# Kernel optimization log

Measured on AMD Instinct MI355X. Metric: run time of the kernel, lower is better.

The kernel has to match this reference:

```python
import jax, jax.numpy as jnp
import numpy as np

D_MODEL = 256
N_LAYERS = 4
D_STATE = 16
EXPAND = 2
D_CONV = 4
D_INNER = EXPAND * D_MODEL
DT_RANK = (D_MODEL + 15) // 16  # ceil(d_model/16) = 16
BATCH = 8
SEQ = 2048
EPS = 1e-5


def setup_inputs() -> dict:
    key = jax.random.key(0)
    ks = jax.random.split(key, 12)
    rn = lambda k, s, sc=0.02: jax.random.normal(k, s, dtype=jnp.float32) * sc
    A_log = jnp.log(jnp.broadcast_to(jnp.arange(1, D_STATE + 1, dtype=jnp.float32),
                                     (N_LAYERS, D_INNER, D_STATE)))
    return {
        "x": jax.random.normal(ks[0], (BATCH, SEQ, 2), dtype=jnp.float32),
        "w_in": rn(ks[1], (D_MODEL, 2), 0.5),
        "b_in": jnp.zeros((D_MODEL,), jnp.float32),
        "norm_w": jnp.ones((N_LAYERS, D_MODEL), jnp.float32),
        "in_proj_w": rn(ks[2], (N_LAYERS, 2 * D_INNER, D_MODEL)),
        "conv_w": rn(ks[3], (N_LAYERS, D_INNER, 1, D_CONV), 0.1),
        "conv_b": jnp.zeros((N_LAYERS, D_INNER), jnp.float32),
        "x_proj_w": rn(ks[4], (N_LAYERS, DT_RANK + 2 * D_STATE, D_INNER)),
        "dt_proj_w": rn(ks[5], (N_LAYERS, D_INNER, DT_RANK), 0.1),
        "dt_proj_b": rn(ks[6], (N_LAYERS, D_INNER), 0.1),
        "A_log": A_log,
        "D_skip": jnp.ones((N_LAYERS, D_INNER), jnp.float32),
        "out_proj_w": rn(ks[7], (N_LAYERS, D_MODEL, D_INNER)),
        "w_head": rn(ks[8], (1, D_MODEL), 0.1),
        "b_head": jnp.zeros((1,), jnp.float32),
    }


def _rmsnorm(x, w):
    return x * jax.lax.rsqrt(jnp.mean(x * x, axis=-1, keepdims=True) + EPS) * w


def _causal_dw_conv(x, w, b):
    # x: (B, L, C); w: (C, 1, K) depthwise; causal left-pad K-1
    xt = jnp.swapaxes(x, 1, 2)  # (B, C, L)
    y = jax.lax.conv_general_dilated(xt, w, (1,), [(D_CONV - 1, 0)],
                                     dimension_numbers=("NCH", "OIH", "NCH"),
                                     feature_group_count=D_INNER)
    return jnp.swapaxes(y + b[None, :, None], 1, 2)


def _selective_scan(u, delta, A, Bm, Cm, Dp):
    # u, delta: (B, L, E); A: (E, N); Bm, Cm: (B, L, N); Dp: (E,)
    dA = jnp.exp(delta[..., None] * A)                 # (B, L, E, N)
    dBu = (delta * u)[..., None] * Bm[:, :, None, :]   # (B, L, E, N)

    def step(h, t):
        dA_t, dBu_t = t
        h = dA_t * h + dBu_t
        return h, h

    h0 = jnp.zeros((u.shape[0], A.shape[0], A.shape[1]), u.dtype)
    _, hs = jax.lax.scan(step, h0, (jnp.swapaxes(dA, 0, 1), jnp.swapaxes(dBu, 0, 1)))
    y = jnp.einsum("lben,bln->ble", hs, Cm)            # (B, L, E)
    return y + u * Dp


def _mamba_block(x, in_w, cw, cb, xp_w, dtw, dtb, A_log, Dp, out_w):
    xz = x @ in_w.T                                    # (B, L, 2E)
    u, z = jnp.split(xz, 2, axis=-1)
    u = jax.nn.silu(_causal_dw_conv(u, cw, cb))
    dbc = u @ xp_w.T                                   # (B, L, dt_rank + 2N)
    delta = jax.nn.softplus(dbc[..., :DT_RANK] @ dtw.T + dtb)
    Bm = dbc[..., DT_RANK:DT_RANK + D_STATE]
    Cm = dbc[..., DT_RANK + D_STATE:]
    y = _selective_scan(u, delta, -jnp.exp(A_log), Bm, Cm, Dp)
    return (y * jax.nn.silu(z)) @ out_w.T


def reference(x, w_in, b_in, norm_w, in_proj_w, conv_w, conv_b, x_proj_w,
              dt_proj_w, dt_proj_b, A_log, D_skip, out_proj_w, w_head, b_head):
    h = x @ w_in.T + b_in                              # (B, L, d_model)
    for i in range(N_LAYERS):
        h = h + _mamba_block(_rmsnorm(h, norm_w[i]), in_proj_w[i], conv_w[i],
                             conv_b[i], x_proj_w[i], dt_proj_w[i], dt_proj_b[i],
                             A_log[i], D_skip[i], out_proj_w[i])
    return (h @ w_head.T + b_head)[..., 0]             # (B, L)
```

## Files before the change

### kernel.cpp

```cpp
#include <hip/hip_runtime.h>
#include <hip/hip_bf16.h>

#define BATCH 8
#define SEQ   2048
#define DM    256
#define DI    512
#define DS    16
#define DTR   16
#define NL    4
#define ROWS  (BATCH*SEQ)
#define NCH   32
#define CHL   64
#define NF    576

typedef __attribute__((ext_vector_type(8))) __bf16 bh8;
typedef __attribute__((ext_vector_type(4))) float f4;

#if __has_builtin(__builtin_amdgcn_exp2f)
#define EXP2(x) __builtin_amdgcn_exp2f(x)
#else
#define EXP2(x) exp2f(x)
#endif
#define LOG2E 1.4426950408889634f

__device__ __forceinline__ float bf2f(unsigned short u) {
    union { unsigned int i; float f; } v; v.i = ((unsigned int)u) << 16; return v.f;
}
__device__ __forceinline__ float4 us4f(ushort4 q) {
    return make_float4(bf2f(q.x), bf2f(q.y), bf2f(q.z), bf2f(q.w));
}
__device__ __forceinline__ float ldg1(const void* p, int i, int bf) {
    if (bf) return bf2f(((const unsigned short*)p)[i]);
    return ((const float*)p)[i];
}
__device__ __forceinline__ float4 ldg4(const void* p, int i, int bf) {
    if (bf) return us4f(*(const ushort4*)(((const unsigned short*)p) + i));
    return *(const float4*)(((const float*)p) + i);
}
__device__ __forceinline__ unsigned short f2bs(float f) {
    union { float f; unsigned u; } x; x.f = f;
    unsigned r = (x.u + 0x7fffu + ((x.u >> 16) & 1u)) >> 16;
    return (unsigned short)r;
}
__device__ __forceinline__ float fsilu(float x) {
    return x * __builtin_amdgcn_rcpf(1.0f + __expf(-x));
}
__device__ __forceinline__ float fsoftplus(float x) {
    return (x > 15.0f) ? x : __logf(1.0f + __expf(x));
}
__device__ __forceinline__ void pow16(float e1, float* pw) {
    float p2 = e1 * e1, p3 = p2 * e1, p4 = p2 * p2;
    float p5 = p4 * e1, p6 = p4 * p2, p7 = p4 * p3, p8 = p4 * p4;
    pw[0] = e1; pw[1] = p2; pw[2] = p3; pw[3] = p4;
    pw[4] = p5; pw[5] = p6; pw[6] = p7; pw[7] = p8;
    pw[8]  = p8 * e1; pw[9]  = p8 * p2; pw[10] = p8 * p3; pw[11] = p8 * p4;
    pw[12] = p8 * p5; pw[13] = p8 * p6; pw[14] = p8 * p7; pw[15] = p8 * p8;
}

typedef const __attribute__((address_space(1))) unsigned int* gas_t;
typedef __attribute__((address_space(3))) unsigned int* las_t;
__device__ __forceinline__ void gl16(const void* g, void* l) {
    __builtin_amdgcn_global_load_lds((gas_t)g, (las_t)l, 16, 0, 0);
}

__global__ void k_probe(const void* x, const void* A_log, int* flag) {
    int t = threadIdx.x;
    float v = bf2f(((const unsigned short*)x)[2 * t]);
    int bad = (fabsf(v) < 32.0f) ? 0 : 1;
    for (int o = 1; o < 64; o <<= 1) bad += __shfl_xor(bad, o);
    int bf = (bad > 8) ? 0 : 1;
    int nb = 0;
    for (int j = 0; j < 64; j++) {
        int e = ((j * 64 + t) * 17) & 32767;
        int n = e & 15;
        float a = ldg1(A_log, e, bf);
        float ea = __expf(a);
        if (fabsf(ea - (float)(n + 1)) > 0.02f * (float)(n + 1)) nb = 1;
    }
    for (int o = 1; o < 64; o <<= 1) nb += __shfl_xor(nb, o);
    if (t == 0) { flag[0] = bf; flag[1] = (nb == 0) ? 1 : 0; }
}

__global__ __launch_bounds__(256) void k_prep(const void* dtw, const void* xpw,
                                              unsigned short* Wc, const int* flag) {
    int bf = *flag;
    int blk = blockIdx.x;
    int l = blk / NF, r = blk % NF;
    int t = threadIdx.x;
    unsigned short* out = Wc + ((size_t)l * NF + r) * DI;
#pragma unroll
    for (int p = 0; p < 2; p++) {
        int k = t + p * 256;
        float v = 0.0f;
        if (r < 512) {
            const int db = l * DI * DTR + r * DTR;
            const int xb = l * 48 * DI;
#pragma unroll
            for (int j = 0; j < 16; j++)
                v = fmaf(ldg1(dtw, db + j, bf), ldg1(xpw, xb + j * DI + k, bf), v);
        } else if (r < 544) {
            v = ldg1(xpw, l * 48 * DI + (16 + r - 512) * DI + k, bf);
        }
        out[k] = f2bs(v);
    }
}

__global__ __launch_bounds__(256) void k_prepw(const void* ipw, const void* norm_w,
                                               unsigned short* Wip, const int* flag) {
    int bf = *flag;
    int blk = blockIdx.x;
    int l = blk >> 10, r = blk & 1023;
    int t = threadIdx.x;
    float v = ldg1(ipw, (l * 1024 + r) * 256 + t, bf) * ldg1(norm_w, l * 256 + t, bf);
    Wip[((size_t)l * 1024 + r) * 256 + t] = f2bs(v);
}

__global__ __launch_bounds__(256) void k_inproj(const void* x, const void* w_in, const void* b_in,
                                                unsigned short* h, float* rssq, const int* flag) {
    int bf = *flag;
    int row = blockIdx.x, e = threadIdx.x;
    float x0 = ldg1(x, row * 2 + 0, bf), x1 = ldg1(x, row * 2 + 1, bf);
    float w0 = ldg1(w_in, e * 2 + 0, bf), w1 = ldg1(w_in, e * 2 + 1, bf);
    float bb = ldg1(b_in, e, bf);
    unsigned short hb = f2bs(fmaf(x0, w0, fmaf(x1, w1, bb)));
    h[(size_t)row * DM + e] = hb;
    float hv = bf2f(hb);
    float ss = hv * hv;
#pragma unroll
    for (int o = 1; o < 64; o <<= 1) ss += __shfl_xor(ss, o);
    if ((e & 63) == 0) rssq[(size_t)row * 4 + (e >> 6)] = ss;
}

#define ASTR 72

template <int BN, bool ADD, bool SCALE, bool RSUM, bool WINT>
__global__ __launch_bounds__(256, 4) void k_mfma(const unsigned short* A, const void* W, int w_off,
                                                 unsigned short* Cp, float* rssq,
                                                 int N, int K, const int* flag) {
    int bf = *flag;
    __shared__ unsigned short SMEM[(128 + BN) * ASTR];
    unsigned short* As = SMEM;
    unsigned short* Ws = SMEM + 128 * 64;
    constexpr int NT = BN / 32;
    constexpr int TSTR = BN + 8;

    int bm = blockIdx.x, bn = blockIdx.y;
    int t = threadIdx.x;
    int w = t >> 6, lane = t & 63;
    int wm = w >> 1, wn = w & 1;
    int lr = lane & 15, quad = lane >> 4;
    int crow = lane >> 3;
    int ccol = ((lane & 7) ^ (lane >> 3)) * 8;

    f4 acc[4][NT];
#pragma unroll
    for (int i = 0; i < 4; i++)
#pragma unroll
        for (int j = 0; j < NT; j++) acc[i][j] = f4{0.f, 0.f, 0.f, 0.f};

    for (int k0 = 0; k0 < K; k0 += 64) {
        __syncthreads();
#pragma unroll
        for (int i = 0; i < 4; i++) {
            int ci = w * 4 + i;
            int r = ci * 8 + crow;
            gl16(A + (size_t)(bm * 128 + r) * K + k0 + ccol, &As[ci * 512]);
        }
        if (WINT || bf) {
#pragma unroll
            for (int i = 0; i < BN / 32; i++) {
                int ci = w * (BN / 32) + i;
                int r = ci * 8 + crow;
                gl16((const unsigned short*)W + (size_t)w_off +
                         (size_t)(bn * BN + r) * K + k0 + ccol,
                     &Ws[ci * 512]);
            }
        } else {
#pragma unroll
            for (int i = 0; i < BN * 8 / 256; i++) {
                int ch = t + i * 256;
                int r = ch >> 3, kc = (ch & 7) * 8;
                size_t off = (size_t)w_off + (size_t)(bn * BN + r) * K + k0 + kc;
                const float* src = (const float*)W + off;
                float4 a0 = *(const float4*)src;
                float4 a1 = *(const float4*)(src + 4);
                ushort4 v0 = { f2bs(a0.x), f2bs(a0.y), f2bs(a0.z), f2bs(a0.w) };
                ushort4 v1 = { f2bs(a1.x), f2bs(a1.y), f2bs(a1.z), f2bs(a1.w) };
                unsigned short* dst = &Ws[r * 64 + (kc ^ ((r & 7) << 3))];
                *(ushort4*)dst = v0;
                *(ushort4*)(dst + 4) = v1;
            }
        }
        __syncthreads();
#pragma unroll
        for (int ks = 0; ks < 64; ks += 32) {
            int csw = (ks + quad * 8) ^ ((lr & 7) << 3);
            bh8 af[4];
#pragma unroll
            for (int i = 0; i < 4; i++)
                af[i] = *(const bh8*)&As[(wm * 64 + i * 16 + lr) * 64 + csw];
            bh8 wf[NT];
#pragma unroll
            for (int j = 0; j < NT; j++)
                wf[j] = *(const bh8*)&Ws[(wn * (BN / 2) + j * 16 + lr) * 64 + csw];
#pragma unroll
            for (int i = 0; i < 4; i++)
#pragma unroll
                for (int j = 0; j < NT; j++)
                    acc[i][j] = __builtin_amdgcn_mfma_f32_16x16x32_bf16(af[i], wf[j], acc[i][j], 0, 0, 0);
        }
    }
    __syncthreads();
    unsigned short* Tile = SMEM;
#pragma unroll
    for (int i = 0; i < 4; i++) {
        int rl = wm * 64 + i * 16 + quad * 4;
        float sc4[4];
        if (SCALE) {
#pragma unroll
            for (int r = 0; r < 4; r++) {
                float4 q4 = *(const float4*)&rssq[(size_t)(bm * 128 + rl + r) * 4];
                sc4[r] = rsqrtf((q4.x + q4.y + q4.z + q4.w) * (1.0f / (float)DM) + 1e-5f);
            }
        }
#pragma unroll
        for (int j = 0; j < NT; j++) {
            int cl = wn * (BN / 2) + j * 16 + lr;
#pragma unroll
            for (int r = 0; r < 4; r++) {
                float vv = acc[i][j][r];
                if (SCALE) vv *= sc4[r];
                Tile[(rl + r) * TSTR + cl] = f2bs(vv);
            }
        }
    }
    __syncthreads();
    constexpr int CPT = 128 * BN / 8 / 256;
#pragma unroll
    for (int i = 0; i < CPT; i++) {
        int ch = t + i * 256;
        int r = ch / (BN / 8), qc = (ch % (BN / 8)) * 8;
        uint4 v = *(uint4*)&Tile[r * TSTR + qc];
        size_t gidx = (size_t)(bm * 128 + r) * N + bn * BN + qc;
        if (ADD) {
            uint4 c = *(uint4*)&Cp[gidx];
            unsigned short* vp = (unsigned short*)&v;
            unsigned short* cp2 = (unsigned short*)&c;
            uint4 ov;
            unsigned short* op = (unsigned short*)&ov;
            float ssq = 0.0f;
#pragma unroll
            for (int e = 0; e < 8; e++) {
                op[e] = f2bs(bf2f(vp[e]) + bf2f(cp2[e]));
                if (RSUM) { float hv = bf2f(op[e]); ssq = fmaf(hv, hv, ssq); }
            }
            *(uint4*)&Cp[gidx] = ov;
            if (RSUM) {
#pragma unroll
                for (int o2 = 1; o2 < 8; o2 <<= 1) ssq += __shfl_xor(ssq, o2);
                if ((lane & 7) == 0) rssq[(size_t)(bm * 128 + r) * 4 + bn] = ssq;
            }
        } else {
            *(uint4*)&Cp[gidx] = v;
        }
    }
}

__global__ __launch_bounds__(256, 4) void k_fused(const unsigned short* A, const unsigned short* Wc,
                                                  int w_off, unsigned short* delta, float* BC,
                                                  const void* dtb, int layer, const int* flag) {
    int bf = *flag;
    __shared__ unsigned short SMEM[(128 + 64) * ASTR];
    unsigned short* As = SMEM;
    unsigned short* Ws = SMEM + 128 * 64;
    constexpr int TSTR = 72;

    int bm = blockIdx.x, bn = blockIdx.y;
    int t = threadIdx.x;
    int w = t >> 6, lane = t & 63;
    int wm = w >> 1, wn = w & 1;
    int lr = lane & 15, quad = lane >> 4;
    int crow = lane >> 3;
    int ccol = ((lane & 7) ^ (lane >> 3)) * 8;

    f4 acc[4][2];
#pragma unroll
    for (int i = 0; i < 4; i++)
#pragma unroll
        for (int j = 0; j < 2; j++) acc[i][j] = f4{0.f, 0.f, 0.f, 0.f};

    for (int k0 = 0; k0 < DI; k0 += 64) {
        __syncthreads();
#pragma unroll
        for (int i = 0; i < 4; i++) {
            int ci = w * 4 + i;
            int r = ci * 8 + crow;
            gl16(A + (size_t)(bm * 128 + r) * DI + k0 + ccol, &As[ci * 512]);
        }
#pragma unroll
        for (int i = 0; i < 2; i++) {
            int ci = w * 2 + i;
            int r = ci * 8 + crow;
            gl16(Wc + (size_t)w_off + (size_t)(bn * 64 + r) * DI + k0 + ccol, &Ws[ci * 512]);
        }
        __syncthreads();
#pragma unroll
        for (int ks = 0; ks < 64; ks += 32) {
            int csw = (ks + quad * 8) ^ ((lr & 7) << 3);
            bh8 af[4];
#pragma unroll
            for (int i = 0; i < 4; i++)
                af[i] = *(const bh8*)&As[(wm * 64 + i * 16 + lr) * 64 + csw];
            bh8 wf[2];
#pragma unroll
            for (int j = 0; j < 2; j++)
                wf[j] = *(const bh8*)&Ws[(wn * 32 + j * 16 + lr) * 64 + csw];
#pragma unroll
            for (int i = 0; i < 4; i++)
#pragma unroll
                for (int j = 0; j < 2; j++)
                    acc[i][j] = __builtin_amdgcn_mfma_f32_16x16x32_bf16(af[i], wf[j], acc[i][j], 0, 0, 0);
        }
    }
    if (bn < 8) {
        __syncthreads();
        unsigned short* Tile = SMEM;
#pragma unroll
        for (int i = 0; i < 4; i++) {
            int rl = wm * 64 + i * 16 + quad * 4;
#pragma unroll
            for (int j = 0; j < 2; j++) {
                int cl = wn * 32 + j * 16 + lr;
                float bb = ldg1(dtb, layer * DI + bn * 64 + cl, bf);
#pragma unroll
                for (int r = 0; r < 4; r++)
                    Tile[(rl + r) * TSTR + cl] = f2bs(fsoftplus(acc[i][j][r] + bb));
            }
        }
        __syncthreads();
#pragma unroll
        for (int i = 0; i < 4; i++) {
            int ch = t + i * 256;
            int r = ch >> 3, qc = (ch & 7) * 8;
            uint4 v = *(uint4*)&Tile[r * TSTR + qc];
            *(uint4*)&delta[(size_t)(bm * 128 + r) * DI + bn * 64 + qc] = v;
        }
    } else {
#pragma unroll
        for (int i = 0; i < 4; i++) {
            int row0 = bm * 128 + wm * 64 + i * 16 + quad * 4;
#pragma unroll
            for (int j = 0; j < 2; j++) {
                int col = bn * 64 + wn * 32 + j * 16 + lr;
                if (col < 544) {
#pragma unroll
                    for (int r = 0; r < 4; r++)
                        BC[(size_t)(row0 + r) * 32 + (col - 512)] = acc[i][j][r];
                }
            }
        }
    }
}

__global__ __launch_bounds__(256) void k_conv(const unsigned short* xz, const void* cw, const void* cb,
                                              int layer, unsigned short* u, const int* flag) {
    int bf = *flag;
    int idx = blockIdx.x * 256 + threadIdx.x;
    int dq = idx & 127;
    int row = idx >> 7;
    int l = row & (SEQ - 1);
    int d = dq * 4;
    float4 w0 = ldg4(cw, (layer * DI + d + 0) * 4, bf);
    float4 w1 = ldg4(cw, (layer * DI + d + 1) * 4, bf);
    float4 w2 = ldg4(cw, (layer * DI + d + 2) * 4, bf);
    float4 w3 = ldg4(cw, (layer * DI + d + 3) * 4, bf);
    float4 bb = ldg4(cb, layer * DI + d, bf);
    const unsigned short* base = xz + (size_t)row * (2 * DI) + d;
    float4 t0 = make_float4(0, 0, 0, 0), t1 = t0, t2 = t0;
    if (l >= 3) t0 = us4f(*(const ushort4*)(base - 3 * 2 * DI));
    if (l >= 2) t1 = us4f(*(const ushort4*)(base - 2 * 2 * DI));
    if (l >= 1) t2 = us4f(*(const ushort4*)(base - 1 * 2 * DI));
    float4 t3 = us4f(*(const ushort4*)base);
    float a0 = bb.x; a0 = fmaf(w0.x, t0.x, a0); a0 = fmaf(w0.y, t1.x, a0); a0 = fmaf(w0.z, t2.x, a0); a0 = fmaf(w0.w, t3.x, a0);
    float a1 = bb.y; a1 = fmaf(w1.x, t0.y, a1); a1 = fmaf(w1.y, t1.y, a1); a1 = fmaf(w1.z, t2.y, a1); a1 = fmaf(w1.w, t3.y, a1);
    float a2 = bb.z; a2 = fmaf(w2.x, t0.z, a2); a2 = fmaf(w2.y, t1.z, a2); a2 = fmaf(w2.z, t2.z, a2); a2 = fmaf(w2.w, t3.z, a2);
    float a3 = bb.w; a3 = fmaf(w3.x, t0.w, a3); a3 = fmaf(w3.y, t1.w, a3); a3 = fmaf(w3.z, t2.w, a3); a3 = fmaf(w3.w, t3.w, a3);
    ushort4 o = { f2bs(fsilu(a0)), f2bs(fsilu(a1)), f2bs(fsilu(a2)), f2bs(fsilu(a3)) };
    *(ushort4*)(u + (size_t)row * DI + d) = o;
}

__global__ __launch_bounds__(256) void k_scan1(const unsigned short* delta, const unsigned short* u,
                                               const float* BC, const void* A_log, float* Sb, float* E,
                                               int layer, const int* flag) {
    int bf = flag[0], sA = flag[1];
    int x = blockIdx.x;
    int dg = x & 1, c = (x >> 1) & (NCH - 1), b = x >> 6;
    int tid = threadIdx.x;
    int d = dg * 256 + tid;
    int t0 = c * CHL;

    __shared__ float sB[CHL][16];
    {
        int r = tid >> 2, q = tid & 3;
        *(float4*)&sB[r][q * 4] =
            *(const float4*)(BC + ((size_t)b * SEQ + t0 + r) * 32 + q * 4);
    }

    float A2[16];
#pragma unroll
    for (int n4 = 0; n4 < 4; n4++) {
        float4 a4 = ldg4(A_log, (layer * DI + d) * DS + n4 * 4, bf);
        A2[n4 * 4 + 0] = -__expf(a4.x) * LOG2E;
        A2[n4 * 4 + 1] = -__expf(a4.y) * LOG2E;
        A2[n4 * 4 + 2] = -__expf(a4.z) * LOG2E;
        A2[n4 * 4 + 3] = -__expf(a4.w) * LOG2E;
    }
    float h[16];
#pragma unroll
    for (int n = 0; n < 16; n++) h[n] = 0.0f;
    float S = 0.0f;

    const unsigned short* dp = delta + ((size_t)b * SEQ + t0) * DI + d;
    const unsigned short* up = u + ((size_t)b * SEQ + t0) * DI + d;

    float dl0[4], uu0[4];
#pragma unroll
    for (int j = 0; j < 4; j++) { dl0[j] = bf2f(dp[j * DI]); uu0[j] = bf2f(up[j * DI]); }
    __syncthreads();

    for (int s = 0; s < CHL / 4; s++) {
        int sn = (s + 1 < CHL / 4) ? (s + 1) : s;
        float dl1[4], uu1[4];
#pragma unroll
        for (int j = 0; j < 4; j++) {
            dl1[j] = bf2f(dp[(sn * 4 + j) * DI]);
            uu1[j] = bf2f(up[(sn * 4 + j) * DI]);
        }
#pragma unroll
        for (int j = 0; j < 4; j++) {
            int t = s * 4 + j;
            float dlt = dl0[j], uu = uu0[j];
            float du = dlt * uu;
            S += dlt;
            if (sA) {
                float pw[16];
                pow16(EXP2(-dlt * LOG2E), pw);
#pragma unroll
                for (int n4 = 0; n4 < 4; n4++) {
                    float4 Bv = *(const float4*)&sB[t][n4 * 4];
                    int n = n4 * 4;
                    h[n + 0] = fmaf(pw[n + 0], h[n + 0], du * Bv.x);
                    h[n + 1] = fmaf(pw[n + 1], h[n + 1], du * Bv.y);
                    h[n + 2] = fmaf(pw[n + 2], h[n + 2], du * Bv.z);
                    h[n + 3] = fmaf(pw[n + 3], h[n + 3], du * Bv.w);
                }
            } else {
#pragma unroll
                for (int n4 = 0; n4 < 4; n4++) {
                    float4 Bv = *(const float4*)&sB[t][n4 * 4];
                    int n = n4 * 4;
                    float a0 = EXP2(dlt * A2[n + 0]); h[n + 0] = fmaf(a0, h[n + 0], du * Bv.x);
                    float a1 = EXP2(dlt * A2[n + 1]); h[n + 1] = fmaf(a1, h[n + 1], du * Bv.y);
                    float a2 = EXP2(dlt * A2[n + 2]); h[n + 2] = fmaf(a2, h[n + 2], du * Bv.z);
                    float a3 = EXP2(dlt * A2[n + 3]); h[n + 3] = fmaf(a3, h[n + 3], du * Bv.w);
                }
            }
        }
#pragma unroll
        for (int j = 0; j < 4; j++) { dl0[j] = dl1[j]; uu0[j] = uu1[j]; }
    }
    Sb[((size_t)b * NCH + c) * DI + d] = S;
    float* Ed = E + (((size_t)b * NCH + c) * DI + d) * DS;
#pragma unroll
    for (int n4 = 0; n4 < 4; n4++)
        *(float4*)(Ed + n4 * 4) = make_float4(h[n4 * 4], h[n4 * 4 + 1], h[n4 * 4 + 2], h[n4 * 4 + 3]);
}

__global__ __launch_bounds__(256) void k_stitch(const float* Sb, const void* A_log, float* E,
                                                int layer, const int* flag) {
    int bf = flag[0];
    int g = blockIdx.x * 256 + threadIdx.x;
    int b = g >> 13, r = g & 8191;
    int d = r >> 4;
    float A2a = -__expf(ldg1(A_log, (layer * DI + d) * DS + (r & 15), bf)) * LOG2E;
    size_t ebase = (size_t)b * NCH * (DI * DS) + r;
    float H = 0.0f;
    for (int c = 0; c < NCH; c++) {
        float p = EXP2(A2a * Sb[((size_t)b * NCH + c) * DI + d]);
        size_t idx = ebase + (size_t)c * (DI * DS);
        float e = E[idx];
        E[idx] = H;
        H = fmaf(p, H, e);
    }
}

__global__ __launch_bounds__(256) void k_scan2(const unsigned short* delta, const unsigned short* u,
                                               const float* BC, const void* A_log, const void* D_skip,
                                               const unsigned short* xz, const float* E,
                                               unsigned short* g, int layer, const int* flag) {
    int bf = flag[0], sA = flag[1];
    int x = blockIdx.x;
    int dg = x & 1, c = (x >> 1) & (NCH - 1), b = x >> 6;
    int tid = threadIdx.x;
    int d = dg * 256 + tid;
    int t0 = c * CHL;

    __shared__ float sBC[CHL][32];
#pragma unroll
    for (int k2 = 0; k2 < 2; k2++) {
        int fi = k2 * 256 + tid;
        int r = fi >> 3, q = fi & 7;
        *(float4*)&sBC[r][q * 4] =
            *(const float4*)(BC + ((size_t)b * SEQ + t0 + r) * 32 + q * 4);
    }

    float A2[16];
#pragma unroll
    for (int n4 = 0; n4 < 4; n4++) {
        float4 a4 = ldg4(A_log, (layer * DI + d) * DS + n4 * 4, bf);
        A2[n4 * 4 + 0] = -__expf(a4.x) * LOG2E;
        A2[n4 * 4 + 1] = -__expf(a4.y) * LOG2E;
        A2[n4 * 4 + 2] = -__expf(a4.z) * LOG2E;
        A2[n4 * 4 + 3] = -__expf(a4.w) * LOG2E;
    }
    float Dp = ldg1(D_skip, layer * DI + d, bf);

    float h[16];
    const float* E0 = E + (((size_t)b * NCH + c) * DI + d) * DS;
#pragma unroll
    for (int n4 = 0; n4 < 4; n4++) {
        float4 h4 = *(const float4*)(E0 + n4 * 4);
        h[n4 * 4 + 0] = h4.x; h[n4 * 4 + 1] = h4.y; h[n4 * 4 + 2] = h4.z; h[n4 * 4 + 3] = h4.w;
    }

    const unsigned short* dp = delta + ((size_t)b * SEQ + t0) * DI + d;
    const unsigned short* up = u + ((size_t)b * SEQ + t0) * DI + d;
    const unsigned short* zp = xz + ((size_t)b * SEQ + t0) * (2 * DI) + DI + d;
    unsigned short* gp = g + ((size_t)b * SEQ + t0) * DI + d;

    float dl0[4], uu0[4], zz0[4];
#pragma unroll
    for (int j = 0; j < 4; j++) {
        dl0[j] = bf2f(dp[j * DI]); uu0[j] = bf2f(up[j * DI]); zz0[j] = bf2f(zp[j * (2 * DI)]);
    }
    __syncthreads();

    for (int s = 0; s < CHL / 4; s++) {
        int sn = (s + 1 < CHL / 4) ? (s + 1) : s;
        float dl1[4], uu1[4], zz1[4];
#pragma unroll
        for (int j = 0; j < 4; j++) {
            dl1[j] = bf2f(dp[(sn * 4 + j) * DI]);
            uu1[j] = bf2f(up[(sn * 4 + j) * DI]);
            zz1[j] = bf2f(zp[(sn * 4 + j) * (2 * DI)]);
        }
#pragma unroll
        for (int j = 0; j < 4; j++) {
            int t = s * 4 + j;
            float dlt = dl0[j], uu = uu0[j], zz = zz0[j];
            float du = dlt * uu;
            float y = 0.0f;
            if (sA) {
                float pw[16];
                pow16(EXP2(-dlt * LOG2E), pw);
#pragma unroll
                for (int n4 = 0; n4 < 4; n4++) {
                    float4 Bv = *(const float4*)&sBC[t][n4 * 4];
                    float4 Cv = *(const float4*)&sBC[t][16 + n4 * 4];
                    int n = n4 * 4;
                    h[n + 0] = fmaf(pw[n + 0], h[n + 0], du * Bv.x); y = fmaf(Cv.x, h[n + 0], y);
                    h[n + 1] = fmaf(pw[n + 1], h[n + 1], du * Bv.y); y = fmaf(Cv.y, h[n + 1], y);
                    h[n + 2] = fmaf(pw[n + 2], h[n + 2], du * Bv.z); y = fmaf(Cv.z, h[n + 2], y);
                    h[n + 3] = fmaf(pw[n + 3], h[n + 3], du * Bv.w); y = fmaf(Cv.w, h[n + 3], y);
                }
            } else {
#pragma unroll
                for (int n4 = 0; n4 < 4; n4++) {
                    float4 Bv = *(const float4*)&sBC[t][n4 * 4];
                    float4 Cv = *(const float4*)&sBC[t][16 + n4 * 4];
                    int n = n4 * 4;
                    float a0 = EXP2(dlt * A2[n + 0]); h[n + 0] = fmaf(a0, h[n + 0], du * Bv.x); y = fmaf(Cv.x, h[n + 0], y);
                    float a1 = EXP2(dlt * A2[n + 1]); h[n + 1] = fmaf(a1, h[n + 1], du * Bv.y); y = fmaf(Cv.y, h[n + 1], y);
                    float a2 = EXP2(dlt * A2[n + 2]); h[n + 2] = fmaf(a2, h[n + 2], du * Bv.z); y = fmaf(Cv.z, h[n + 2], y);
                    float a3 = EXP2(dlt * A2[n + 3]); h[n + 3] = fmaf(a3, h[n + 3], du * Bv.w); y = fmaf(Cv.w, h[n + 3], y);
                }
            }
            float yt = fmaf(uu, Dp, y);
            gp[(size_t)t * DI] = f2bs(yt * fsilu(zz));
        }
#pragma unroll
        for (int j = 0; j < 4; j++) { dl0[j] = dl1[j]; uu0[j] = uu1[j]; zz0[j] = zz1[j]; }
    }
}

__global__ __launch_bounds__(256) void k_head(const unsigned short* h, const void* w_head,
                                              const void* b_head, void* out, const int* flag) {
    int bf = *flag;
    int wv = threadIdx.x >> 6, ln = threadIdx.x & 63;
    int row = blockIdx.x * 4 + wv;
    float4 v = us4f(*(const ushort4*)(h + (size_t)row * DM + ln * 4));
    float4 w = ldg4(w_head, ln * 4, bf);
    float s = v.x * w.x + v.y * w.y + v.z * w.z + v.w * w.w;
    for (int o = 1; o < 64; o <<= 1) s += __shfl_xor(s, o);
    if (ln == 0) {
        s += ldg1(b_head, 0, bf);
        if (bf) ((__hip_bfloat16*)out)[row] = __float2bfloat16(s);
        else    ((float*)out)[row] = s;
    }
}

extern "C" void kernel_launch(void* const* d_in, const int* in_sizes, int n_in,
                              void* d_out, int out_size, void* d_ws, size_t ws_size,
                              hipStream_t stream) {
    (void)in_sizes; (void)n_in; (void)out_size; (void)ws_size;
    const void* x      = d_in[0];
    const void* w_in   = d_in[1];
    const void* b_in   = d_in[2];
    const void* norm_w = d_in[3];
    const void* ipw    = d_in[4];
    const void* cw     = d_in[5];
    const void* cb     = d_in[6];
    const void* xpw    = d_in[7];
    const void* dtw    = d_in[8];
    const void* dtb    = d_in[9];
    const void* A_log  = d_in[10];
    const void* D_skip = d_in[11];
    const void* opw    = d_in[12];
    const void* w_head = d_in[13];
    const void* b_head = d_in[14];

    float* ws    = (float*)d_ws;
    unsigned short* h     = (unsigned short*)ws;
    float*          rssq  = ws + 4194304;
    float*          Sb    = ws + 4194304;
    float*          E     = ws + 4718592;
    unsigned short* xz    = (unsigned short*)(ws + 8388608);
    unsigned short* u     = (unsigned short*)(ws + 25165824);
    float*          BC    = ws + 33554432;
    unsigned short* delta = (unsigned short*)(ws + 34340864);
    unsigned short* Wcomb = (unsigned short*)(ws + 38535168);
    unsigned short* Wipc  = (unsigned short*)(ws + 39124992);
    int*            flag  = (int*)(ws + 42729472);

    k_probe<<<1, 64, 0, stream>>>(x, A_log, flag);
    k_prep<<<NL * NF, 256, 0, stream>>>(dtw, xpw, Wcomb, flag);
    k_prepw<<<NL * 1024, 256, 0, stream>>>(ipw, norm_w, Wipc, flag);
    k_inproj<<<ROWS, 256, 0, stream>>>(x, w_in, b_in, h, rssq, flag);

    for (int layer = 0; layer < NL; layer++) {
        k_mfma<128, false, true, false, true><<<dim3(ROWS / 128, 2 * DI / 128), 256, 0, stream>>>(
            h, Wipc, layer * 2 * DI * DM, xz, rssq, 2 * DI, DM, flag);
        k_conv<<<ROWS * DI / 4 / 256, 256, 0, stream>>>(xz, cw, cb, layer, u, flag);
        k_fused<<<dim3(ROWS / 128, NF / 64), 256, 0, stream>>>(
            u, Wcomb, layer * NF * DI, delta, BC, dtb, layer, flag);
        k_scan1<<<BATCH * NCH * 2, 256, 0, stream>>>(delta, u, BC, A_log, Sb, E, layer, flag);
        k_stitch<<<BATCH * DI * DS / 256, 256, 0, stream>>>(Sb, A_log, E, layer, flag);
        k_scan2<<<BATCH * NCH * 2, 256, 0, stream>>>(delta, u, BC, A_log, D_skip, xz, E,
                                                     u , layer, flag);
        k_mfma<64, true, false, true, false><<<dim3(ROWS / 128, DM / 64), 256, 0, stream>>>(
            u, opw, layer * DM * DI, h, rssq, DM, DI, flag);
    }

    k_head<<<ROWS / 4, 256, 0, stream>>>(h, w_head, b_head, d_out, flag);
}
```

Measured before the change: 587.7 us.

## Fuse causal conv into in-projection GEMM and fold chunk stitch into scan2

The in-projection GEMM now computes the u-half tiles together with 16 extra halo rows, normalizes them with rssq, and applies the depthwise causal conv plus SiLU from shared memory. This removes the separate k_conv pass that re-read xz. The k_stitch kernel is also removed, and each scan2 block recomputes its own starting state by serially combining the earlier chunks' summaries. This costs redundant halo MFMAs and an O(c) prefix loop per block, which is quadratic in chunk count over the whole grid, in exchange for two fewer launches and less global traffic.

```diff
diff --git a/kernel.cpp b/kernel.cpp
--- a/kernel.cpp
+++ b/kernel.cpp
@@ -133,6 +133,155 @@
 
 #define ASTR 72
 
+__global__ __launch_bounds__(256, 4) void k_ipconv(const unsigned short* A, const unsigned short* W,
+                                                   int w_off, unsigned short* xz, unsigned short* u,
+                                                   const float* rssq, const void* cw, const void* cb,
+                                                   int layer, const int* flag) {
+    int bf = *flag;
+    constexpr int K = DM;
+    constexpr int TSTR = 136;
+    __shared__ unsigned short SMEM[144 * TSTR];
+    unsigned short* As  = SMEM;
+    unsigned short* As2 = SMEM + 8192;
+    unsigned short* Ws  = SMEM + 9216;
+
+    int bm = blockIdx.x, bn = blockIdx.y;
+    bool ublk = (bn < 4);
+    int t = threadIdx.x;
+    int w = t >> 6, lane = t & 63;
+    int wm = w >> 1, wn = w & 1;
+    int lr = lane & 15, quad = lane >> 4;
+    int crow = lane >> 3;
+    int ccol = ((lane & 7) ^ (lane >> 3)) * 8;
+
+    f4 acc[4][4];
+    f4 acc5[4];
+#pragma unroll
+    for (int i = 0; i < 4; i++) {
+        acc5[i] = f4{0.f, 0.f, 0.f, 0.f};
+#pragma unroll
+        for (int j = 0; j < 4; j++) acc[i][j] = f4{0.f, 0.f, 0.f, 0.f};
+    }
+
+    for (int k0 = 0; k0 < K; k0 += 64) {
+        __syncthreads();
+#pragma unroll
+        for (int i = 0; i < 4; i++) {
+            int ci = w * 4 + i;
+            int r = ci * 8 + crow;
+            gl16(A + (size_t)(bm * 128 + r) * K + k0 + ccol, &As[ci * 512]);
+        }
+        if (ublk && w < 2) {
+            int rg = bm * 128 - 16 + w * 8 + crow;
+            if (rg < 0) rg = 0;
+            gl16(A + (size_t)rg * K + k0 + ccol, &As2[w * 512]);
+        }
+#pragma unroll
+        for (int i = 0; i < 4; i++) {
+            int ci = w * 4 + i;
+            int r = ci * 8 + crow;
+            gl16(W + (size_t)w_off + (size_t)(bn * 128 + r) * K + k0 + ccol, &Ws[ci * 512]);
+        }
+        __syncthreads();
+#pragma unroll
+        for (int ks = 0; ks < 64; ks += 32) {
+            int csw = (ks + quad * 8) ^ ((lr & 7) << 3);
+            bh8 af[4];
+#pragma unroll
+            for (int i = 0; i < 4; i++)
+                af[i] = *(const bh8*)&As[(wm * 64 + i * 16 + lr) * 64 + csw];
+            bh8 wf[4];
+#pragma unroll
+            for (int j = 0; j < 4; j++)
+                wf[j] = *(const bh8*)&Ws[(wn * 64 + j * 16 + lr) * 64 + csw];
+#pragma unroll
+            for (int i = 0; i < 4; i++)
+#pragma unroll
+                for (int j = 0; j < 4; j++)
+                    acc[i][j] = __builtin_amdgcn_mfma_f32_16x16x32_bf16(af[i], wf[j], acc[i][j], 0, 0, 0);
+            if (ublk && wm == 0) {
+                bh8 a5 = *(const bh8*)&As2[lr * 64 + csw];
+#pragma unroll
+                for (int j = 0; j < 4; j++)
+                    acc5[j] = __builtin_amdgcn_mfma_f32_16x16x32_bf16(a5, wf[j], acc5[j], 0, 0, 0);
+            }
+        }
+    }
+    __syncthreads();
+    unsigned short* Tile = SMEM;
+#pragma unroll
+    for (int i = 0; i < 4; i++) {
+        int rl = wm * 64 + i * 16 + quad * 4;
+        float sc4[4];
+#pragma unroll
+        for (int r = 0; r < 4; r++) {
+            float4 q4 = *(const float4*)&rssq[(size_t)(bm * 128 + rl + r) * 4];
+            sc4[r] = rsqrtf((q4.x + q4.y + q4.z + q4.w) * (1.0f / (float)DM) + 1e-5f);
+        }
+#pragma unroll
+        for (int j = 0; j < 4; j++) {
+            int cl = wn * 64 + j * 16 + lr;
+#pragma unroll
+            for (int r = 0; r < 4; r++)
+                Tile[(rl + r) * TSTR + cl] = f2bs(acc[i][j][r] * sc4[r]);
+        }
+    }
+    if (ublk && wm == 0) {
+#pragma unroll
+        for (int r = 0; r < 4; r++) {
+            int er = quad * 4 + r;
+            int rg = bm * 128 - 16 + er;
+            if (rg < 0) rg = 0;
+            float4 q4 = *(const float4*)&rssq[(size_t)rg * 4];
+            float sc = rsqrtf((q4.x + q4.y + q4.z + q4.w) * (1.0f / (float)DM) + 1e-5f);
+#pragma unroll
+            for (int j = 0; j < 4; j++) {
+                int cl = wn * 64 + j * 16 + lr;
+                Tile[(128 + er) * TSTR + cl] = f2bs(acc5[j][r] * sc);
+            }
+        }
+    }
+    __syncthreads();
+    if (!ublk) {
+#pragma unroll
+        for (int i = 0; i < 8; i++) {
+            int ch = t + i * 256;
+            int r = ch >> 4, qc = (ch & 15) * 8;
+            uint4 v = *(uint4*)&Tile[r * TSTR + qc];
+            *(uint4*)&xz[(size_t)(bm * 128 + r) * 1024 + bn * 128 + qc] = v;
+        }
+    } else {
+        int col4 = t & 31, rowg = t >> 5;
+        int c0 = col4 * 4;
+        int dg = bn * 128 + c0;
+        float4 wv0 = ldg4(cw, (layer * DI + dg + 0) * 4, bf);
+        float4 wv1 = ldg4(cw, (layer * DI + dg + 1) * 4, bf);
+        float4 wv2 = ldg4(cw, (layer * DI + dg + 2) * 4, bf);
+        float4 wv3 = ldg4(cw, (layer * DI + dg + 3) * 4, bf);
+        float4 bb = ldg4(cb, layer * DI + dg, bf);
+        bool bstart = ((bm & 15) == 0);
+        int r0 = rowg * 16;
+        auto ldrow = [&](int q) -> float4 {
+            if (q < 0) {
+                if (bstart) return make_float4(0.f, 0.f, 0.f, 0.f);
+                return us4f(*(const ushort4*)&Tile[(144 + q) * TSTR + c0]);
+            }
+            return us4f(*(const ushort4*)&Tile[q * TSTR + c0]);
+        };
+        float4 xm3 = ldrow(r0 - 3), xm2 = ldrow(r0 - 2), xm1 = ldrow(r0 - 1);
+        for (int rr = r0; rr < r0 + 16; rr++) {
+            float4 x0 = us4f(*(const ushort4*)&Tile[rr * TSTR + c0]);
+            float a0 = bb.x; a0 = fmaf(wv0.x, xm3.x, a0); a0 = fmaf(wv0.y, xm2.x, a0); a0 = fmaf(wv0.z, xm1.x, a0); a0 = fmaf(wv0.w, x0.x, a0);
+            float a1 = bb.y; a1 = fmaf(wv1.x, xm3.y, a1); a1 = fmaf(wv1.y, xm2.y, a1); a1 = fmaf(wv1.z, xm1.y, a1); a1 = fmaf(wv1.w, x0.y, a1);
+            float a2 = bb.z; a2 = fmaf(wv2.x, xm3.z, a2); a2 = fmaf(wv2.y, xm2.z, a2); a2 = fmaf(wv2.z, xm1.z, a2); a2 = fmaf(wv2.w, x0.z, a2);
+            float a3 = bb.w; a3 = fmaf(wv3.x, xm3.w, a3); a3 = fmaf(wv3.y, xm2.w, a3); a3 = fmaf(wv3.z, xm1.w, a3); a3 = fmaf(wv3.w, x0.w, a3);
+            ushort4 o = { f2bs(fsilu(a0)), f2bs(fsilu(a1)), f2bs(fsilu(a2)), f2bs(fsilu(a3)) };
+            *(ushort4*)&u[(size_t)(bm * 128 + rr) * DI + dg] = o;
+            xm3 = xm2; xm2 = xm1; xm1 = x0;
+        }
+    }
+}
+
 template <int BN, bool ADD, bool SCALE, bool RSUM, bool WINT>
 __global__ __launch_bounds__(256, 4) void k_mfma(const unsigned short* A, const void* W, int w_off,
                                                  unsigned short* Cp, float* rssq,
@@ -362,33 +511,6 @@
     }
 }
 
-__global__ __launch_bounds__(256) void k_conv(const unsigned short* xz, const void* cw, const void* cb,
-                                              int layer, unsigned short* u, const int* flag) {
-    int bf = *flag;
-    int idx = blockIdx.x * 256 + threadIdx.x;
-    int dq = idx & 127;
-    int row = idx >> 7;
-    int l = row & (SEQ - 1);
-    int d = dq * 4;
-    float4 w0 = ldg4(cw, (layer * DI + d + 0) * 4, bf);
-    float4 w1 = ldg4(cw, (layer * DI + d + 1) * 4, bf);
-    float4 w2 = ldg4(cw, (layer * DI + d + 2) * 4, bf);
-    float4 w3 = ldg4(cw, (layer * DI + d + 3) * 4, bf);
-    float4 bb = ldg4(cb, layer * DI + d, bf);
-    const unsigned short* base = xz + (size_t)row * (2 * DI) + d;
-    float4 t0 = make_float4(0, 0, 0, 0), t1 = t0, t2 = t0;
-    if (l >= 3) t0 = us4f(*(const ushort4*)(base - 3 * 2 * DI));
-    if (l >= 2) t1 = us4f(*(const ushort4*)(base - 2 * 2 * DI));
-    if (l >= 1) t2 = us4f(*(const ushort4*)(base - 1 * 2 * DI));
-    float4 t3 = us4f(*(const ushort4*)base);
-    float a0 = bb.x; a0 = fmaf(w0.x, t0.x, a0); a0 = fmaf(w0.y, t1.x, a0); a0 = fmaf(w0.z, t2.x, a0); a0 = fmaf(w0.w, t3.x, a0);
-    float a1 = bb.y; a1 = fmaf(w1.x, t0.y, a1); a1 = fmaf(w1.y, t1.y, a1); a1 = fmaf(w1.z, t2.y, a1); a1 = fmaf(w1.w, t3.y, a1);
-    float a2 = bb.z; a2 = fmaf(w2.x, t0.z, a2); a2 = fmaf(w2.y, t1.z, a2); a2 = fmaf(w2.z, t2.z, a2); a2 = fmaf(w2.w, t3.z, a2);
-    float a3 = bb.w; a3 = fmaf(w3.x, t0.w, a3); a3 = fmaf(w3.y, t1.w, a3); a3 = fmaf(w3.z, t2.w, a3); a3 = fmaf(w3.w, t3.w, a3);
-    ushort4 o = { f2bs(fsilu(a0)), f2bs(fsilu(a1)), f2bs(fsilu(a2)), f2bs(fsilu(a3)) };
-    *(ushort4*)(u + (size_t)row * DI + d) = o;
-}
-
 __global__ __launch_bounds__(256) void k_scan1(const unsigned short* delta, const unsigned short* u,
                                                const float* BC, const void* A_log, float* Sb, float* E,
                                                int layer, const int* flag) {
@@ -476,27 +598,9 @@
         *(float4*)(Ed + n4 * 4) = make_float4(h[n4 * 4], h[n4 * 4 + 1], h[n4 * 4 + 2], h[n4 * 4 + 3]);
 }
 
-__global__ __launch_bounds__(256) void k_stitch(const float* Sb, const void* A_log, float* E,
-                                                int layer, const int* flag) {
-    int bf = flag[0];
-    int g = blockIdx.x * 256 + threadIdx.x;
-    int b = g >> 13, r = g & 8191;
-    int d = r >> 4;
-    float A2a = -__expf(ldg1(A_log, (layer * DI + d) * DS + (r & 15), bf)) * LOG2E;
-    size_t ebase = (size_t)b * NCH * (DI * DS) + r;
-    float H = 0.0f;
-    for (int c = 0; c < NCH; c++) {
-        float p = EXP2(A2a * Sb[((size_t)b * NCH + c) * DI + d]);
-        size_t idx = ebase + (size_t)c * (DI * DS);
-        float e = E[idx];
-        E[idx] = H;
-        H = fmaf(p, H, e);
-    }
-}
-
 __global__ __launch_bounds__(256) void k_scan2(const unsigned short* delta, const unsigned short* u,
                                                const float* BC, const void* A_log, const void* D_skip,
-                                               const unsigned short* xz, const float* E,
+                                               const unsigned short* xz, const float* Sb, const float* E,
                                                unsigned short* g, int layer, const int* flag) {
     int bf = flag[0], sA = flag[1];
     int x = blockIdx.x;
@@ -526,11 +630,34 @@
     float Dp = ldg1(D_skip, layer * DI + d, bf);
 
     float h[16];
-    const float* E0 = E + (((size_t)b * NCH + c) * DI + d) * DS;
-#pragma unroll
-    for (int n4 = 0; n4 < 4; n4++) {
-        float4 h4 = *(const float4*)(E0 + n4 * 4);
-        h[n4 * 4 + 0] = h4.x; h[n4 * 4 + 1] = h4.y; h[n4 * 4 + 2] = h4.z; h[n4 * 4 + 3] = h4.w;
+#pragma unroll
+    for (int n = 0; n < 16; n++) h[n] = 0.0f;
+    for (int cc = 0; cc < c; cc++) {
+        float S = Sb[((size_t)b * NCH + cc) * DI + d];
+        const float* Ep = E + (((size_t)b * NCH + cc) * DI + d) * DS;
+        if (sA) {
+            float pw[16];
+            pow16(EXP2(-S * LOG2E), pw);
+#pragma unroll
+            for (int n4 = 0; n4 < 4; n4++) {
+                float4 e4 = *(const float4*)(Ep + n4 * 4);
+                int n = n4 * 4;
+                h[n + 0] = fmaf(pw[n + 0], h[n + 0], e4.x);
+                h[n + 1] = fmaf(pw[n + 1], h[n + 1], e4.y);
+                h[n + 2] = fmaf(pw[n + 2], h[n + 2], e4.z);
+                h[n + 3] = fmaf(pw[n + 3], h[n + 3], e4.w);
+            }
+        } else {
+#pragma unroll
+            for (int n4 = 0; n4 < 4; n4++) {
+                float4 e4 = *(const float4*)(Ep + n4 * 4);
+                int n = n4 * 4;
+                h[n + 0] = fmaf(EXP2(A2[n + 0] * S), h[n + 0], e4.x);
+                h[n + 1] = fmaf(EXP2(A2[n + 1] * S), h[n + 1], e4.y);
+                h[n + 2] = fmaf(EXP2(A2[n + 2] * S), h[n + 2], e4.z);
+                h[n + 3] = fmaf(EXP2(A2[n + 3] * S), h[n + 3], e4.w);
+            }
+        }
     }
 
     const unsigned short* dp = delta + ((size_t)b * SEQ + t0) * DI + d;
@@ -648,14 +775,12 @@
     k_inproj<<<ROWS, 256, 0, stream>>>(x, w_in, b_in, h, rssq, flag);
 
     for (int layer = 0; layer < NL; layer++) {
-        k_mfma<128, false, true, false, true><<<dim3(ROWS / 128, 2 * DI / 128), 256, 0, stream>>>(
-            h, Wipc, layer * 2 * DI * DM, xz, rssq, 2 * DI, DM, flag);
-        k_conv<<<ROWS * DI / 4 / 256, 256, 0, stream>>>(xz, cw, cb, layer, u, flag);
+        k_ipconv<<<dim3(ROWS / 128, 8), 256, 0, stream>>>(
+            h, Wipc, layer * 2 * DI * DM, xz, u, rssq, cw, cb, layer, flag);
         k_fused<<<dim3(ROWS / 128, NF / 64), 256, 0, stream>>>(
             u, Wcomb, layer * NF * DI, delta, BC, dtb, layer, flag);
         k_scan1<<<BATCH * NCH * 2, 256, 0, stream>>>(delta, u, BC, A_log, Sb, E, layer, flag);
-        k_stitch<<<BATCH * DI * DS / 256, 256, 0, stream>>>(Sb, A_log, E, layer, flag);
-        k_scan2<<<BATCH * NCH * 2, 256, 0, stream>>>(delta, u, BC, A_log, D_skip, xz, E,
+        k_scan2<<<BATCH * NCH * 2, 256, 0, stream>>>(delta, u, BC, A_log, D_skip, xz, Sb, E,
                                                      u , layer, flag);
         k_mfma<64, true, false, true, false><<<dim3(ROWS / 128, DM / 64), 256, 0, stream>>>(
             u, opw, layer * DM * DI, h, rssq, DM, DI, flag);
```

Measured after the change: 604.2 us. 1.03x slower.
